# Performance work log

Hardware: AMD Instinct MI355X
Metric: run time of the kernel (lower is better)

Reference implementation:

```python
import jax, jax.numpy as jnp
import numpy as np

B, S, D = 4, 2048, 1024
NEG = 1e9


def setup_inputs() -> dict:
    key = jax.random.key(0)
    ks = jax.random.split(key, 4)
    scale = 1.0 / np.sqrt(D)  # glorot-ish init scale for stability
    x = jax.random.normal(ks[0], (B, S, D), dtype=jnp.float32)
    Wq = jax.random.normal(ks[1], (D, D), dtype=jnp.float32) * scale
    Wk = jax.random.normal(ks[2], (D, D), dtype=jnp.float32) * scale
    Wv = jax.random.normal(ks[3], (D, D), dtype=jnp.float32) * scale
    bq = jnp.zeros((D,), jnp.float32)
    bk = jnp.zeros((D,), jnp.float32)
    bv = jnp.zeros((D,), jnp.float32)
    return {"x": x, "Wq": Wq, "bq": bq, "Wk": Wk, "bk": bk, "Wv": Wv, "bv": bv}


def reference(x, Wq, bq, Wk, bk, Wv, bv):
    # Dense projections (single head, no 1/sqrt(d) scaling, matching source)
    q = x @ Wq + bq                      # [B,S,D]
    k = x @ Wk + bk                      # [B,S,D]
    v = x @ Wv + bv                      # [B,S,D]
    scores = jnp.einsum('bqd,bkd->bqk', q, k)   # [B,S,S]
    seq = scores.shape[-1]
    mask = jnp.tril(jnp.ones((seq, seq), scores.dtype))  # lower-triangular causal
    scores = scores * mask - NEG * (1.0 - mask)
    weights = jax.nn.softmax(scores, axis=-1)
    return jnp.einsum('bqk,bkd->bqd', weights, v)
```

## Files before the change

kernel.cpp:

```cpp
#include <hip/hip_runtime.h>

typedef float f32x4  __attribute__((ext_vector_type(4)));
typedef _Float16 f16x8  __attribute__((ext_vector_type(8)));
typedef _Float16 f16x4v __attribute__((ext_vector_type(4)));
typedef _Float16 f16x8v __attribute__((ext_vector_type(8)));

__device__ inline void load_lds16(const _Float16* g, _Float16* l) {
    __builtin_amdgcn_global_load_lds((const __attribute__((address_space(1))) void*)g,
                                     (__attribute__((address_space(3))) void*)l, 16, 0, 0);
}

__global__ __launch_bounds__(256)
void convert_h(const float* __restrict__ X, _Float16* __restrict__ H, long n4)
{
    long i = (long)blockIdx.x * 256 + threadIdx.x;
    if (i >= n4) return;
    f32x4 v = ((const f32x4*)X)[i];
    f16x4v h;
#pragma unroll
    for (int k = 0; k < 4; ++k) h[k] = (_Float16)v[k];
    ((f16x4v*)H)[i] = h;
}

__global__ __launch_bounds__(256)
void transpose_w3(const float* __restrict__ Wq, const float* __restrict__ Wk,
                  const float* __restrict__ Wv,
                  _Float16* __restrict__ W2, _Float16* __restrict__ Wvt, int D)
{
    const int z = blockIdx.z;
    const float* W = (z == 0) ? Wq : (z == 1) ? Wk : Wv;

    __shared__ float t[32][33];
    const int tid = threadIdx.x;
    const int bx = blockIdx.x * 32, by = blockIdx.y * 32;
    const int c = tid & 31, r0 = tid >> 5;
#pragma unroll
    for (int r = r0; r < 32; r += 8)
        t[r][c] = W[(long)(by + r) * D + bx + c];
    __syncthreads();
#pragma unroll
    for (int r = r0; r < 32; r += 8) {
        float v = t[c][r];
        _Float16 h = (_Float16)v;
        if (z < 2) {
            const long nrow = (long)z * D + bx + r;
            W2[nrow * 2 * D + by + c]     = h;
            W2[nrow * 2 * D + D + by + c] = (_Float16)(v - (float)h);
        } else {
            Wvt[(long)(bx + r) * D + by + c] = h;
        }
    }
}

__global__ __launch_bounds__(512)
void proj8(const _Float16* __restrict__ x_h, const _Float16* __restrict__ W2,
           const _Float16* __restrict__ Wvt,
           _Float16* __restrict__ Q_h, _Float16* __restrict__ K_h,
           _Float16* __restrict__ K_l, _Float16* __restrict__ Vt,
           const float* __restrict__ bq, const float* __restrict__ bk,
           const float* __restrict__ bv)
{
    constexpr int D = 1024, SEQ = 2048;
    __shared__ __align__(16) _Float16 lds[65536];

    const int orig = blockIdx.x;
    const bool isV = orig >= 256;
    int ct, rt, ldb, NT2;
    const _Float16* Bb;
    if (!isV) {
        const int x = orig & 7, i = orig >> 3;
        rt = x * 4 + (i & 3);  ct = i >> 2;
        Bb = W2;  ldb = 2 * D; NT2 = 64;
    } else {
        const int o = orig - 256, x = o & 7, i = o >> 3;
        rt = x * 4 + (i & 3);  ct = i >> 2;
        Bb = Wvt; ldb = D;     NT2 = 32;
    }
    const int row0 = rt * 256, col0 = ct * 256;

    const int tid = threadIdx.x;
    const int wave = tid >> 6, lane = tid & 63, l16 = lane & 15, quad = lane >> 4;
    const int wmh = (wave >> 2) * 128;
    const int wn  = (wave & 3) * 64;
    const int ahalf = (wave >> 2) << 2;

#define STAGES(gb, ld, base0, kbase, dst)                                       \
    {                                                                           \
        _Pragma("unroll")                                                       \
        for (int q_ = 0; q_ < 2; ++q_) {                                        \
            const int p_ = q_ * 512 + tid;                                      \
            const int rp_ = p_ >> 3;                                            \
            const int gl_ = (p_ & 7) ^ (rp_ & 7);                               \
            const int row_ = rp_ + ((gl_ >> 2) << 7);                           \
            load_lds16((gb) + (long)((base0) + row_) * (ld) + (kbase) +         \
                           ((gl_ & 3) << 3),                                    \
                       (dst) + p_ * 8);                                         \
        }                                                                       \
    }

    STAGES(x_h, D, row0, 0,  lds);
    STAGES(Bb, ldb, col0, 0, lds + 32768);
    STAGES(x_h, D, row0, 32, lds + 8192);
    STAGES(Bb, ldb, col0, 32, lds + 32768 + 8192);
    asm volatile("s_waitcnt vmcnt(4)" ::: "memory");
    __builtin_amdgcn_s_barrier();

    f32x4 acc[8][4] = {};

    for (int s = 0; s < NT2; ++s) {
        _Float16* Asl = lds + (s & 3) * 8192;
        _Float16* Bsl = lds + 32768 + (s & 3) * 8192;
        const bool pf = (s + 2 < NT2);
        const int kA2 = ((s + 2) * 32) & (D - 1);
        const int kB2 = (s + 2) * 32;

        f16x8 b[4], a0[4];
#pragma unroll
        for (int j = 0; j < 4; ++j) {
            const int nr = wn + j * 16 + l16;
            const int rpb = nr & 127;
            const int gpb = ((((nr >> 7) << 2) | quad) ^ (rpb & 7));
            b[j] = *(const f16x8*)&Bsl[rpb * 64 + gpb * 8];
        }
#pragma unroll
        for (int il = 0; il < 4; ++il) {
            const int rp = il * 16 + l16;
            const int gpa = ((ahalf | quad) ^ (rp & 7));
            a0[il] = *(const f16x8*)&Asl[rp * 64 + gpa * 8];
        }
        if (pf) STAGES(x_h, D, row0, kA2, lds + ((s + 2) & 3) * 8192);
        __builtin_amdgcn_s_setprio(1);
#pragma unroll
        for (int il = 0; il < 4; ++il)
#pragma unroll
            for (int j = 0; j < 4; ++j)
                acc[il][j] = __builtin_amdgcn_mfma_f32_16x16x32_f16(
                    a0[il], b[j], acc[il][j], 0, 0, 0);
        __builtin_amdgcn_s_setprio(0);

        f16x8 a1[4];
#pragma unroll
        for (int il = 0; il < 4; ++il) {
            const int rp = (il + 4) * 16 + l16;
            const int gpa = ((ahalf | quad) ^ (rp & 7));
            a1[il] = *(const f16x8*)&Asl[rp * 64 + gpa * 8];
        }
        if (pf) STAGES(Bb, ldb, col0, kB2, lds + 32768 + ((s + 2) & 3) * 8192);
        __builtin_amdgcn_s_setprio(1);
#pragma unroll
        for (int il = 0; il < 4; ++il)
#pragma unroll
            for (int j = 0; j < 4; ++j)
                acc[4 + il][j] = __builtin_amdgcn_mfma_f32_16x16x32_f16(
                    a1[il], b[j], acc[4 + il][j], 0, 0, 0);
        __builtin_amdgcn_s_setprio(0);

        if (pf)                asm volatile("s_waitcnt vmcnt(4)" ::: "memory");
        else if (s + 2 == NT2) asm volatile("s_waitcnt vmcnt(0)" ::: "memory");
        __builtin_amdgcn_s_barrier();
    }

    if (!isV) {
        const bool isQ = ct < 4;
        const float* bias = isQ ? bq : bk;
#pragma unroll
        for (int j = 0; j < 4; ++j) {
            const int colg = col0 + wn + j * 16 + l16;
            const int cc = isQ ? colg : colg - D;
            const float bval = bias[cc];
#pragma unroll
            for (int i = 0; i < 8; ++i) {
                const int rb = row0 + wmh + i * 16 + quad * 4;
#pragma unroll
                for (int r = 0; r < 4; ++r) {
                    const float v = acc[i][j][r] + bval;
                    const _Float16 h = (_Float16)v;
                    if (isQ) {
                        Q_h[(long)(rb + r) * D + cc] = h;
                    } else {
                        K_h[(long)(rb + r) * D + cc] = h;
                        K_l[(long)(rb + r) * D + cc] = (_Float16)(v - (float)h);
                    }
                }
            }
        }
    } else {
        _Float16* sVt = lds;
#pragma unroll
        for (int j = 0; j < 4; ++j) {
            const int cl = wn + j * 16 + l16;
            const float bval = bv[col0 + cl];
#pragma unroll
            for (int i = 0; i < 8; ++i) {
                f16x4v pk;
#pragma unroll
                for (int r = 0; r < 4; ++r) pk[r] = (_Float16)(acc[i][j][r] + bval);
                const int rowb = wmh * 2 + i * 32 + quad * 8;
                const int sb = cl * 512 + (rowb ^ ((cl & 31) << 4));
                *(f16x4v*)((char*)sVt + sb) = pk;
            }
        }
        __syncthreads();
        const int bb = row0 >> 11;
        const int s0 = row0 & (SEQ - 1);
        for (int idx = tid; idx < 8192; idx += 512) {
            const int cl = idx >> 5, r8 = idx & 31;
            const int sb = cl * 512 + ((r8 * 16) ^ ((cl & 31) << 4));
            f16x8v v = *(const f16x8v*)&((char*)sVt)[sb];
            *(f16x8v*)&Vt[((long)bb * D + col0 + cl) * SEQ + s0 + r8 * 8] = v;
        }
    }
#undef STAGES
}

constexpr int TM = 128, TK = 32;

template<bool BLO, int MODE, int TNB>
__global__ __launch_bounds__(256)
void gemm2(const _Float16* __restrict__ Ah, long sA, int lda,
           const _Float16* __restrict__ Bh, const _Float16* __restrict__ Bl,
           long sB, int ldb,
           float* __restrict__ Cf, long sC, int ldc, int K)
{
    static_assert(MODE != 1 || TNB == 64, "packed causal decode assumes TNB=64");
    constexpr int NFJ = TNB / 32;
    constexpr int BRNDS = TNB / 64;

    int rt, ct;
    if (MODE == 1) {
        const int t = blockIdx.x;
        rt = (int)((sqrtf(4.0f * t + 1.0f) - 1.0f) * 0.5f);
        while (rt * (rt + 1) > t) --rt;
        while ((rt + 1) * (rt + 2) <= t) ++rt;
        ct = t - rt * (rt + 1);
    } else {
        rt = (gridDim.x - 1) - blockIdx.x;
        ct = blockIdx.y;
    }
    const int bz = blockIdx.z;

    const _Float16* gAh = Ah + (long)bz * sA;
    const _Float16* gBh = Bh + (long)bz * sB;
    const _Float16* gBl = BLO ? Bl + (long)bz * sB : nullptr;

    const int row0 = rt * TM, col0 = ct * TNB;
    const int k_end = (MODE == 2) ? min(K, (rt + 1) * TM) : K;

    __shared__ _Float16 sAh[TM * TK];
    __shared__ _Float16 sBh[TNB * TK];
    __shared__ _Float16 sBl[BLO ? TNB * TK : 8];

    const int tid = threadIdx.x;
    const int lane = tid & 63, wave = tid >> 6;
    const int l16 = lane & 15, quad = lane >> 4;
    const int wm = (wave >> 1) * 64, wn = (wave & 1) * (TNB / 2);

    f32x4 acc[4][NFJ] = {};

    for (int k0 = 0; k0 < k_end; k0 += TK) {
#pragma unroll
        for (int rnd = 0; rnd < 2; ++rnd) {
            const int row = rnd * 64 + (tid >> 2);
            const long gA = (long)(row0 + row) * lda + k0 + (tid & 3) * 8;
            load_lds16(gAh + gA, sAh + rnd * 2048 + tid * 8);
        }
#pragma unroll
        for (int rnd = 0; rnd < BRNDS; ++rnd) {
            const int row = rnd * 64 + (tid >> 2);
            const long gB = (long)(col0 + row) * ldb + k0 + (tid & 3) * 8;
            const int lofs = rnd * 2048 + tid * 8;
            load_lds16(gBh + gB, sBh + lofs);
            if (BLO) load_lds16(gBl + gB, sBl + lofs);
        }
        __syncthreads();

        f16x8 a[4], b_h[NFJ];
#pragma unroll
        for (int i = 0; i < 4; ++i)
            a[i] = *(const f16x8*)&sAh[(wm + i * 16 + l16) * TK + (quad << 3)];
#pragma unroll
        for (int j = 0; j < NFJ; ++j)
            b_h[j] = *(const f16x8*)&sBh[(wn + j * 16 + l16) * TK + (quad << 3)];

        if (BLO) {
            f16x8 b_l[NFJ];
#pragma unroll
            for (int j = 0; j < NFJ; ++j)
                b_l[j] = *(const f16x8*)&sBl[(wn + j * 16 + l16) * TK + (quad << 3)];
#pragma unroll
            for (int i = 0; i < 4; ++i)
#pragma unroll
                for (int j = 0; j < NFJ; ++j) {
                    acc[i][j] = __builtin_amdgcn_mfma_f32_16x16x32_f16(a[i], b_h[j], acc[i][j], 0, 0, 0);
                    acc[i][j] = __builtin_amdgcn_mfma_f32_16x16x32_f16(a[i], b_l[j], acc[i][j], 0, 0, 0);
                }
        } else {
#pragma unroll
            for (int i = 0; i < 4; ++i)
#pragma unroll
                for (int j = 0; j < NFJ; ++j)
                    acc[i][j] = __builtin_amdgcn_mfma_f32_16x16x32_f16(a[i], b_h[j], acc[i][j], 0, 0, 0);
        }
        __syncthreads();
    }

    float* cf = Cf + (long)bz * sC;
#pragma unroll
    for (int j = 0; j < NFJ; ++j) {
        const int col = col0 + wn + j * 16 + l16;
#pragma unroll
        for (int i = 0; i < 4; ++i) {
            const int rb = row0 + wm + i * 16 + quad * 4;
#pragma unroll
            for (int r = 0; r < 4; ++r)
                cf[(long)(rb + r) * ldc + col] = acc[i][j][r];
        }
    }
}

__global__ __launch_bounds__(256)
void softmax_kernel(const float* __restrict__ Sc, _Float16* __restrict__ P, int seq)
{
    const int r = blockIdx.x, b = blockIdx.y;
    const float* row = Sc + ((long)b * seq + r) * seq;
    _Float16* prow = P + ((long)b * seq + r) * seq;
    const int tid = threadIdx.x;
    const int cmax = ((r >> 7) + 1) << 7;
    const int c0 = tid * 8;

    float v[8];
    f32x4 v0, v1;
    if (c0 <= r) {
        const f32x4* rp = (const f32x4*)row;
        v0 = rp[tid * 2];
        v1 = rp[tid * 2 + 1];
    } else {
        v0 = (f32x4)(-3.0e38f);
        v1 = (f32x4)(-3.0e38f);
    }
    float lmax = -3.0e38f;
#pragma unroll
    for (int k = 0; k < 4; ++k) {
        v[k]     = (c0 + k     <= r) ? v0[k] : -3.0e38f;
        v[k + 4] = (c0 + k + 4 <= r) ? v1[k] : -3.0e38f;
    }
#pragma unroll
    for (int k = 0; k < 8; ++k) lmax = fmaxf(lmax, v[k]);

    __shared__ float red[256];
    red[tid] = lmax; __syncthreads();
    for (int s = 128; s > 0; s >>= 1) {
        if (tid < s) red[tid] = fmaxf(red[tid], red[tid + s]);
        __syncthreads();
    }
    const float m = red[0];
    __syncthreads();

    float lsum = 0.0f;
#pragma unroll
    for (int k = 0; k < 8; ++k) {
        float e = (v[k] > -1.0e38f) ? __expf(v[k] - m) : 0.0f;
        v[k] = e;
        lsum += e;
    }
    red[tid] = lsum; __syncthreads();
    for (int s = 128; s > 0; s >>= 1) {
        if (tid < s) red[tid] += red[tid + s];
        __syncthreads();
    }
    const float inv = 1.0f / red[0];

    if (c0 < cmax) {
        f16x8v o;
#pragma unroll
        for (int k = 0; k < 8; ++k) o[k] = (_Float16)(v[k] * inv);
        ((f16x8v*)prow)[tid] = o;
    }
}

extern "C" void kernel_launch(void* const* d_in, const int* in_sizes, int n_in,
                              void* d_out, int out_size, void* d_ws, size_t ws_size,
                              hipStream_t stream)
{
    constexpr int B = 4, S = 2048, D = 1024;
    constexpr long MB = 1024 * 1024;
    const float* x  = (const float*)d_in[0];
    const float* Wq = (const float*)d_in[1];
    const float* bq = (const float*)d_in[2];
    const float* Wk = (const float*)d_in[3];
    const float* bk = (const float*)d_in[4];
    const float* Wv = (const float*)d_in[5];
    const float* bv = (const float*)d_in[6];
    float* out = (float*)d_out;

    char* ws = (char*)d_ws;
    _Float16* x_h   = (_Float16*)(ws + 0);
    _Float16* W2    = (_Float16*)(ws + 16 * MB);
    _Float16* Wvt_h = (_Float16*)(ws + 24 * MB);
    float*    Sc    = (float*)(ws + 0);
    _Float16* Q_h   = (_Float16*)(ws + 64 * MB);
    _Float16* K_h   = (_Float16*)(ws + 80 * MB);
    _Float16* K_l   = (_Float16*)(ws + 96 * MB);
    _Float16* Vt    = (_Float16*)(ws + 112 * MB);
    _Float16* P     = (_Float16*)(ws + 128 * MB);

    const int M = B * S;
    dim3 blk(256);

    convert_h<<<(M * D / 4 + 255) / 256, blk, 0, stream>>>(x, x_h, (long)M * D / 4);
    transpose_w3<<<dim3(D / 32, D / 32, 3), blk, 0, stream>>>(
        Wq, Wk, Wv, W2, Wvt_h, D);

    proj8<<<dim3(384), dim3(512), 0, stream>>>(
        x_h, W2, Wvt_h, Q_h, K_h, K_l, Vt, bq, bk, bv);

    const int ntiles = (S / TM) * (S / TM + 1);
    gemm2<true, 1, 64><<<dim3(ntiles, 1, B), blk, 0, stream>>>(
        Q_h, (long)S * D, D, K_h, K_l, (long)S * D, D,
        Sc, (long)S * S, S, D);

    softmax_kernel<<<dim3(S, B), blk, 0, stream>>>(Sc, P, S);

    gemm2<false, 2, 64><<<dim3(S / TM, D / 64, B), blk, 0, stream>>>(
        P, (long)S * S, S, Vt, nullptr, (long)D * S, S,
        out, (long)S * D, D, S);
}
```

Baseline: 334.7 us.

## Replace generic score and PV GEMMs with large-tile pipelined kernels

Interleaves K high and low halves into one row-contiguous buffer so the Q·K score GEMM becomes a single K=2048 GEMM. That GEMM uses the same 256x256, 512-thread, 4-stage LDS-pipelined MFMA kernel as the projection, over a causal lower-triangular tile list. The P·V GEMM gets a dedicated 256x128 pipelined kernel with a causal k-range. The softmax mask extent is widened to 256 to match the new tile granularity. This is meant to raise operand reuse and overlap loads with MFMA, at the cost of fewer blocks (36 per batch for scores) and less causal skipping at coarser tiles.

```diff
diff --git a/kernel.cpp b/kernel.cpp
--- a/kernel.cpp
+++ b/kernel.cpp
@@ -52,11 +52,25 @@
     }
 }
 
+#define STAGES_T(NTHR, NQ, gb, ld, base0, kbase, dst)                           \
+    {                                                                           \
+        _Pragma("unroll")                                                       \
+        for (int q_ = 0; q_ < (NQ); ++q_) {                                     \
+            const int p_ = q_ * (NTHR) + tid;                                   \
+            const int rp_ = p_ >> 3;                                            \
+            const int gl_ = (p_ & 7) ^ (rp_ & 7);                               \
+            const int row_ = rp_ + ((gl_ >> 2) << 7);                           \
+            load_lds16((gb) + (long)((base0) + row_) * (ld) + (kbase) +         \
+                           ((gl_ & 3) << 3),                                    \
+                       (dst) + p_ * 8);                                         \
+        }                                                                       \
+    }
+
 __global__ __launch_bounds__(512)
 void proj8(const _Float16* __restrict__ x_h, const _Float16* __restrict__ W2,
            const _Float16* __restrict__ Wvt,
-           _Float16* __restrict__ Q_h, _Float16* __restrict__ K_h,
-           _Float16* __restrict__ K_l, _Float16* __restrict__ Vt,
+           _Float16* __restrict__ Q_h, _Float16* __restrict__ Khl,
+           _Float16* __restrict__ Vt,
            const float* __restrict__ bq, const float* __restrict__ bk,
            const float* __restrict__ bv)
 {
@@ -84,24 +98,10 @@
     const int wn  = (wave & 3) * 64;
     const int ahalf = (wave >> 2) << 2;
 
-#define STAGES(gb, ld, base0, kbase, dst)                                       \
-    {                                                                           \
-        _Pragma("unroll")                                                       \
-        for (int q_ = 0; q_ < 2; ++q_) {                                        \
-            const int p_ = q_ * 512 + tid;                                      \
-            const int rp_ = p_ >> 3;                                            \
-            const int gl_ = (p_ & 7) ^ (rp_ & 7);                               \
-            const int row_ = rp_ + ((gl_ >> 2) << 7);                           \
-            load_lds16((gb) + (long)((base0) + row_) * (ld) + (kbase) +         \
-                           ((gl_ & 3) << 3),                                    \
-                       (dst) + p_ * 8);                                         \
-        }                                                                       \
-    }
-
-    STAGES(x_h, D, row0, 0,  lds);
-    STAGES(Bb, ldb, col0, 0, lds + 32768);
-    STAGES(x_h, D, row0, 32, lds + 8192);
-    STAGES(Bb, ldb, col0, 32, lds + 32768 + 8192);
+    STAGES_T(512, 2, x_h, D, row0, 0,  lds);
+    STAGES_T(512, 2, Bb, ldb, col0, 0, lds + 32768);
+    STAGES_T(512, 2, x_h, D, row0, 32, lds + 8192);
+    STAGES_T(512, 2, Bb, ldb, col0, 32, lds + 32768 + 8192);
     asm volatile("s_waitcnt vmcnt(4)" ::: "memory");
     __builtin_amdgcn_s_barrier();
 
@@ -128,7 +128,7 @@
             const int gpa = ((ahalf | quad) ^ (rp & 7));
             a0[il] = *(const f16x8*)&Asl[rp * 64 + gpa * 8];
         }
-        if (pf) STAGES(x_h, D, row0, kA2, lds + ((s + 2) & 3) * 8192);
+        if (pf) STAGES_T(512, 2, x_h, D, row0, kA2, lds + ((s + 2) & 3) * 8192);
         __builtin_amdgcn_s_setprio(1);
 #pragma unroll
         for (int il = 0; il < 4; ++il)
@@ -145,7 +145,7 @@
             const int gpa = ((ahalf | quad) ^ (rp & 7));
             a1[il] = *(const f16x8*)&Asl[rp * 64 + gpa * 8];
         }
-        if (pf) STAGES(Bb, ldb, col0, kB2, lds + 32768 + ((s + 2) & 3) * 8192);
+        if (pf) STAGES_T(512, 2, Bb, ldb, col0, kB2, lds + 32768 + ((s + 2) & 3) * 8192);
         __builtin_amdgcn_s_setprio(1);
 #pragma unroll
         for (int il = 0; il < 4; ++il)
@@ -178,8 +178,8 @@
                     if (isQ) {
                         Q_h[(long)(rb + r) * D + cc] = h;
                     } else {
-                        K_h[(long)(rb + r) * D + cc] = h;
-                        K_l[(long)(rb + r) * D + cc] = (_Float16)(v - (float)h);
+                        Khl[(long)(rb + r) * 2048 + cc] = h;
+                        Khl[(long)(rb + r) * 2048 + 1024 + cc] = (_Float16)(v - (float)h);
                     }
                 }
             }
@@ -210,112 +210,204 @@
             *(f16x8v*)&Vt[((long)bb * D + col0 + cl) * SEQ + s0 + r8 * 8] = v;
         }
     }
-#undef STAGES
-}
-
-constexpr int TM = 128, TK = 32;
-
-template<bool BLO, int MODE, int TNB>
+}
+
+__global__ __launch_bounds__(512)
+void gemm_sc(const _Float16* __restrict__ Q, const _Float16* __restrict__ Khl,
+             float* __restrict__ Sc)
+{
+    constexpr int D = 1024, S = 2048;
+    __shared__ __align__(16) _Float16 lds[65536];
+
+    const int bz = blockIdx.y;
+    const int t = blockIdx.x;
+    int rt = (int)((sqrtf(8.0f * t + 1.0f) - 1.0f) * 0.5f);
+    while (rt * (rt + 1) / 2 > t) --rt;
+    while ((rt + 1) * (rt + 2) / 2 <= t) ++rt;
+    const int ct = t - rt * (rt + 1) / 2;
+
+    const _Float16* gA = Q + (long)bz * S * D;
+    const _Float16* gB = Khl + (long)bz * S * 2048;
+    const int row0 = rt * 256, col0 = ct * 256;
+    constexpr int NT2 = 64;
+
+    const int tid = threadIdx.x;
+    const int wave = tid >> 6, lane = tid & 63, l16 = lane & 15, quad = lane >> 4;
+    const int wmh = (wave >> 2) * 128;
+    const int wn  = (wave & 3) * 64;
+    const int ahalf = (wave >> 2) << 2;
+
+    STAGES_T(512, 2, gA, D, row0, 0,  lds);
+    STAGES_T(512, 2, gB, 2048, col0, 0, lds + 32768);
+    STAGES_T(512, 2, gA, D, row0, 32, lds + 8192);
+    STAGES_T(512, 2, gB, 2048, col0, 32, lds + 32768 + 8192);
+    asm volatile("s_waitcnt vmcnt(4)" ::: "memory");
+    __builtin_amdgcn_s_barrier();
+
+    f32x4 acc[8][4] = {};
+
+    for (int s = 0; s < NT2; ++s) {
+        _Float16* Asl = lds + (s & 3) * 8192;
+        _Float16* Bsl = lds + 32768 + (s & 3) * 8192;
+        const bool pf = (s + 2 < NT2);
+        const int kA2 = ((s + 2) * 32) & (D - 1);
+        const int kB2 = (s + 2) * 32;
+
+        f16x8 b[4], a0[4];
+#pragma unroll
+        for (int j = 0; j < 4; ++j) {
+            const int nr = wn + j * 16 + l16;
+            const int rpb = nr & 127;
+            const int gpb = ((((nr >> 7) << 2) | quad) ^ (rpb & 7));
+            b[j] = *(const f16x8*)&Bsl[rpb * 64 + gpb * 8];
+        }
+#pragma unroll
+        for (int il = 0; il < 4; ++il) {
+            const int rp = il * 16 + l16;
+            const int gpa = ((ahalf | quad) ^ (rp & 7));
+            a0[il] = *(const f16x8*)&Asl[rp * 64 + gpa * 8];
+        }
+        if (pf) STAGES_T(512, 2, gA, D, row0, kA2, lds + ((s + 2) & 3) * 8192);
+        __builtin_amdgcn_s_setprio(1);
+#pragma unroll
+        for (int il = 0; il < 4; ++il)
+#pragma unroll
+            for (int j = 0; j < 4; ++j)
+                acc[il][j] = __builtin_amdgcn_mfma_f32_16x16x32_f16(
+                    a0[il], b[j], acc[il][j], 0, 0, 0);
+        __builtin_amdgcn_s_setprio(0);
+
+        f16x8 a1[4];
+#pragma unroll
+        for (int il = 0; il < 4; ++il) {
+            const int rp = (il + 4) * 16 + l16;
+            const int gpa = ((ahalf | quad) ^ (rp & 7));
+            a1[il] = *(const f16x8*)&Asl[rp * 64 + gpa * 8];
+        }
+        if (pf) STAGES_T(512, 2, gB, 2048, col0, kB2, lds + 32768 + ((s + 2) & 3) * 8192);
+        __builtin_amdgcn_s_setprio(1);
+#pragma unroll
+        for (int il = 0; il < 4; ++il)
+#pragma unroll
+            for (int j = 0; j < 4; ++j)
+                acc[4 + il][j] = __builtin_amdgcn_mfma_f32_16x16x32_f16(
+                    a1[il], b[j], acc[4 + il][j], 0, 0, 0);
+        __builtin_amdgcn_s_setprio(0);
+
+        if (pf)                asm volatile("s_waitcnt vmcnt(4)" ::: "memory");
+        else if (s + 2 == NT2) asm volatile("s_waitcnt vmcnt(0)" ::: "memory");
+        __builtin_amdgcn_s_barrier();
+    }
+
+    float* cf = Sc + (long)bz * S * S;
+#pragma unroll
+    for (int j = 0; j < 4; ++j) {
+        const int col = col0 + wn + j * 16 + l16;
+#pragma unroll
+        for (int i = 0; i < 8; ++i) {
+            const int rb = row0 + wmh + i * 16 + quad * 4;
+#pragma unroll
+            for (int r = 0; r < 4; ++r)
+                cf[(long)(rb + r) * S + col] = acc[i][j][r];
+        }
+    }
+}
+
 __global__ __launch_bounds__(256)
-void gemm2(const _Float16* __restrict__ Ah, long sA, int lda,
-           const _Float16* __restrict__ Bh, const _Float16* __restrict__ Bl,
-           long sB, int ldb,
-           float* __restrict__ Cf, long sC, int ldc, int K)
-{
-    static_assert(MODE != 1 || TNB == 64, "packed causal decode assumes TNB=64");
-    constexpr int NFJ = TNB / 32;
-    constexpr int BRNDS = TNB / 64;
-
-    int rt, ct;
-    if (MODE == 1) {
-        const int t = blockIdx.x;
-        rt = (int)((sqrtf(4.0f * t + 1.0f) - 1.0f) * 0.5f);
-        while (rt * (rt + 1) > t) --rt;
-        while ((rt + 1) * (rt + 2) <= t) ++rt;
-        ct = t - rt * (rt + 1);
-    } else {
-        rt = (gridDim.x - 1) - blockIdx.x;
-        ct = blockIdx.y;
-    }
+void gemm_pv(const _Float16* __restrict__ P, const _Float16* __restrict__ Vt,
+             float* __restrict__ Out)
+{
+    constexpr int D = 1024, S = 2048;
+    __shared__ __align__(16) _Float16 lds[49152];
+
+    const int rt = 7 - (int)blockIdx.x;
+    const int ct = blockIdx.y;
     const int bz = blockIdx.z;
-
-    const _Float16* gAh = Ah + (long)bz * sA;
-    const _Float16* gBh = Bh + (long)bz * sB;
-    const _Float16* gBl = BLO ? Bl + (long)bz * sB : nullptr;
-
-    const int row0 = rt * TM, col0 = ct * TNB;
-    const int k_end = (MODE == 2) ? min(K, (rt + 1) * TM) : K;
-
-    __shared__ _Float16 sAh[TM * TK];
-    __shared__ _Float16 sBh[TNB * TK];
-    __shared__ _Float16 sBl[BLO ? TNB * TK : 8];
+    const _Float16* gA = P + (long)bz * S * S;
+    const _Float16* gB = Vt + (long)bz * D * S;
+    const int row0 = rt * 256, col0 = ct * 128;
+    const int NT2 = (rt + 1) * 8;
 
     const int tid = threadIdx.x;
-    const int lane = tid & 63, wave = tid >> 6;
-    const int l16 = lane & 15, quad = lane >> 4;
-    const int wm = (wave >> 1) * 64, wn = (wave & 1) * (TNB / 2);
-
-    f32x4 acc[4][NFJ] = {};
-
-    for (int k0 = 0; k0 < k_end; k0 += TK) {
-#pragma unroll
-        for (int rnd = 0; rnd < 2; ++rnd) {
-            const int row = rnd * 64 + (tid >> 2);
-            const long gA = (long)(row0 + row) * lda + k0 + (tid & 3) * 8;
-            load_lds16(gAh + gA, sAh + rnd * 2048 + tid * 8);
-        }
-#pragma unroll
-        for (int rnd = 0; rnd < BRNDS; ++rnd) {
-            const int row = rnd * 64 + (tid >> 2);
-            const long gB = (long)(col0 + row) * ldb + k0 + (tid & 3) * 8;
-            const int lofs = rnd * 2048 + tid * 8;
-            load_lds16(gBh + gB, sBh + lofs);
-            if (BLO) load_lds16(gBl + gB, sBl + lofs);
-        }
-        __syncthreads();
-
-        f16x8 a[4], b_h[NFJ];
-#pragma unroll
-        for (int i = 0; i < 4; ++i)
-            a[i] = *(const f16x8*)&sAh[(wm + i * 16 + l16) * TK + (quad << 3)];
-#pragma unroll
-        for (int j = 0; j < NFJ; ++j)
-            b_h[j] = *(const f16x8*)&sBh[(wn + j * 16 + l16) * TK + (quad << 3)];
-
-        if (BLO) {
-            f16x8 b_l[NFJ];
-#pragma unroll
-            for (int j = 0; j < NFJ; ++j)
-                b_l[j] = *(const f16x8*)&sBl[(wn + j * 16 + l16) * TK + (quad << 3)];
-#pragma unroll
-            for (int i = 0; i < 4; ++i)
-#pragma unroll
-                for (int j = 0; j < NFJ; ++j) {
-                    acc[i][j] = __builtin_amdgcn_mfma_f32_16x16x32_f16(a[i], b_h[j], acc[i][j], 0, 0, 0);
-                    acc[i][j] = __builtin_amdgcn_mfma_f32_16x16x32_f16(a[i], b_l[j], acc[i][j], 0, 0, 0);
-                }
-        } else {
-#pragma unroll
-            for (int i = 0; i < 4; ++i)
-#pragma unroll
-                for (int j = 0; j < NFJ; ++j)
-                    acc[i][j] = __builtin_amdgcn_mfma_f32_16x16x32_f16(a[i], b_h[j], acc[i][j], 0, 0, 0);
-        }
-        __syncthreads();
-    }
-
-    float* cf = Cf + (long)bz * sC;
-#pragma unroll
-    for (int j = 0; j < NFJ; ++j) {
+    const int wave = tid >> 6, lane = tid & 63, l16 = lane & 15, quad = lane >> 4;
+    const int wmh = (wave >> 1) * 128;
+    const int wn  = (wave & 1) * 64;
+    const int ahalf = (wave >> 1) << 2;
+
+#define STAGEB_PV(kbase, dst)                                                   \
+    {                                                                           \
+        _Pragma("unroll")                                                       \
+        for (int q_ = 0; q_ < 2; ++q_) {                                        \
+            const int p_ = q_ * 256 + tid;                                      \
+            const int rp_ = p_ >> 3;                                            \
+            const int gl_ = (p_ & 7) ^ (rp_ & 7);                               \
+            const int row_ = rp_ + ((gl_ >> 2) << 6);                           \
+            load_lds16(gB + (long)(col0 + row_) * S + (kbase) +                 \
+                           ((gl_ & 3) << 3),                                    \
+                       (dst) + p_ * 8);                                         \
+        }                                                                       \
+    }
+
+    STAGES_T(256, 4, gA, S, row0, 0,  lds);
+    STAGEB_PV(0, lds + 32768);
+    STAGES_T(256, 4, gA, S, row0, 32, lds + 8192);
+    STAGEB_PV(32, lds + 32768 + 4096);
+    asm volatile("s_waitcnt vmcnt(6)" ::: "memory");
+    __builtin_amdgcn_s_barrier();
+
+    f32x4 acc[8][4] = {};
+
+    for (int s = 0; s < NT2; ++s) {
+        _Float16* Asl = lds + (s & 3) * 8192;
+        _Float16* Bsl = lds + 32768 + (s & 3) * 4096;
+        const bool pf = (s + 2 < NT2);
+        const int k2 = (s + 2) * 32;
+
+        f16x8 b[4], a[8];
+#pragma unroll
+        for (int j = 0; j < 4; ++j) {
+            const int nr = wn + j * 16 + l16;
+            const int rpb = nr & 63;
+            const int gpb = ((((nr >> 6) << 2) | quad) ^ (rpb & 7));
+            b[j] = *(const f16x8*)&Bsl[rpb * 64 + gpb * 8];
+        }
+#pragma unroll
+        for (int il = 0; il < 8; ++il) {
+            const int rp = il * 16 + l16;
+            const int gpa = ((ahalf | quad) ^ (rp & 7));
+            a[il] = *(const f16x8*)&Asl[rp * 64 + gpa * 8];
+        }
+        if (pf) {
+            STAGES_T(256, 4, gA, S, row0, k2, lds + ((s + 2) & 3) * 8192);
+            STAGEB_PV(k2, lds + 32768 + ((s + 2) & 3) * 4096);
+        }
+        __builtin_amdgcn_s_setprio(1);
+#pragma unroll
+        for (int il = 0; il < 8; ++il)
+#pragma unroll
+            for (int j = 0; j < 4; ++j)
+                acc[il][j] = __builtin_amdgcn_mfma_f32_16x16x32_f16(
+                    a[il], b[j], acc[il][j], 0, 0, 0);
+        __builtin_amdgcn_s_setprio(0);
+
+        if (pf)                asm volatile("s_waitcnt vmcnt(6)" ::: "memory");
+        else if (s + 2 == NT2) asm volatile("s_waitcnt vmcnt(0)" ::: "memory");
+        __builtin_amdgcn_s_barrier();
+    }
+
+    float* cf = Out + (long)bz * S * D;
+#pragma unroll
+    for (int j = 0; j < 4; ++j) {
         const int col = col0 + wn + j * 16 + l16;
 #pragma unroll
-        for (int i = 0; i < 4; ++i) {
-            const int rb = row0 + wm + i * 16 + quad * 4;
+        for (int i = 0; i < 8; ++i) {
+            const int rb = row0 + wmh + i * 16 + quad * 4;
 #pragma unroll
             for (int r = 0; r < 4; ++r)
-                cf[(long)(rb + r) * ldc + col] = acc[i][j][r];
-        }
-    }
+                cf[(long)(rb + r) * D + col] = acc[i][j][r];
+        }
+    }
+#undef STAGEB_PV
 }
 
 __global__ __launch_bounds__(256)
@@ -325,7 +417,7 @@
     const float* row = Sc + ((long)b * seq + r) * seq;
     _Float16* prow = P + ((long)b * seq + r) * seq;
     const int tid = threadIdx.x;
-    const int cmax = ((r >> 7) + 1) << 7;
+    const int cmax = ((r >> 8) + 1) << 8;
     const int c0 = tid * 8;
 
     float v[8];
@@ -399,8 +491,7 @@
     _Float16* Wvt_h = (_Float16*)(ws + 24 * MB);
     float*    Sc    = (float*)(ws + 0);
     _Float16* Q_h   = (_Float16*)(ws + 64 * MB);
-    _Float16* K_h   = (_Float16*)(ws + 80 * MB);
-    _Float16* K_l   = (_Float16*)(ws + 96 * MB);
+    _Float16* Khl   = (_Float16*)(ws + 80 * MB);
     _Float16* Vt    = (_Float16*)(ws + 112 * MB);
     _Float16* P     = (_Float16*)(ws + 128 * MB);
 
@@ -412,16 +503,11 @@
         Wq, Wk, Wv, W2, Wvt_h, D);
 
     proj8<<<dim3(384), dim3(512), 0, stream>>>(
-        x_h, W2, Wvt_h, Q_h, K_h, K_l, Vt, bq, bk, bv);
-
-    const int ntiles = (S / TM) * (S / TM + 1);
-    gemm2<true, 1, 64><<<dim3(ntiles, 1, B), blk, 0, stream>>>(
-        Q_h, (long)S * D, D, K_h, K_l, (long)S * D, D,
-        Sc, (long)S * S, S, D);
+        x_h, W2, Wvt_h, Q_h, Khl, Vt, bq, bk, bv);
+
+    gemm_sc<<<dim3(36, B), dim3(512), 0, stream>>>(Q_h, Khl, Sc);
 
     softmax_kernel<<<dim3(S, B), blk, 0, stream>>>(Sc, P, S);
 
-    gemm2<false, 2, 64><<<dim3(S / TM, D / 64, B), blk, 0, stream>>>(
-        P, (long)S * S, S, Vt, nullptr, (long)D * S, S,
-        out, (long)S * D, D, S);
-}
+    gemm_pv<<<dim3(8, 8, B), dim3(256), 0, stream>>>(P, Vt, out);
+}
```

Result: faster. 317.6 us (-5.1%).
